# Optimization experiments

Measured on AMD Instinct MI355X. Metric: run time of the kernel, lower is better.

## Reference

```python
import jax, jax.numpy as jnp
import numpy as np
from functools import partial

# ---- constants from params ----
NODES = 64          # cfg_s[0]: nodes per graph
HEADS, BASES = 8, 4 # EGConv num_heads / num_bases (aggregators = ['symnorm'], A=1)
THRESH, LENS = 0.5, 0.5
ENC_THRESH, ENC_LENS = 0.5, 0.5
DECAY = 0.2
LSTM_ALPHA = 2.0

# ---- surrogate spike functions ----
@partial(jax.custom_vjp, nondiff_argnums=(1, 2))
def atan_spike(x, thresh, alpha):
    return (x > thresh).astype(x.dtype)

def _atan_fwd(x, thresh, alpha):
    return atan_spike(x, thresh, alpha), x

def _atan_bwd(thresh, alpha, x, g):
    grad = (alpha / 2.0) / (1.0 + (jnp.pi / 2.0 * alpha * (x - thresh)) ** 2)
    return (g * grad,)

atan_spike.defvjp(_atan_fwd, _atan_bwd)

@partial(jax.custom_vjp, nondiff_argnums=(1,))
def erf_spike(x, alpha):
    return (x > 0).astype(x.dtype)

def _erf_fwd(x, alpha):
    return erf_spike(x, alpha), x

def _erf_bwd(alpha, x, g):
    grad = alpha / (2.0 * jnp.sqrt(jnp.pi)) * jnp.exp(-(alpha * x / 2.0) ** 2)
    return (g * grad,)

erf_spike.defvjp(_erf_fwd, _erf_bwd)


def setup_inputs() -> dict:
    key = jax.random.key(0)
    N, Cin, T = 16384, 8, 32
    Cenc, Cgnn = 128, 128
    Fh = Cgnn // HEADS
    HID, FC1, NC = 512, 256, 4
    E = 262144
    ks = jax.random.split(key, 12)

    def w(k, shape, fan_in):
        return jax.random.normal(k, shape, jnp.float32) / np.float32(np.sqrt(fan_in))

    return {
        "x": jax.random.normal(ks[0], (N, Cin, T), jnp.float32),
        "edge_index": jax.random.randint(ks[1], (2, E), 0, N, dtype=jnp.int32),
        "enc_W": w(ks[2], (Cin, Cenc), Cin),
        "enc_b": jnp.zeros((Cenc,), jnp.float32),
        "bases_W": w(ks[3], (Cenc, BASES * Fh), Cenc),
        "bases_b": jnp.zeros((BASES * Fh,), jnp.float32),
        "comb_W": w(ks[4], (Cenc, HEADS * BASES), Cenc),
        "comb_b": jnp.zeros((HEADS * BASES,), jnp.float32),
        "conv_bias": jnp.zeros((Cgnn,), jnp.float32),
        "W_ih": w(ks[5], (NODES * Cgnn, 4 * HID), NODES * Cgnn),
        "W_hh": w(ks[6], (HID, 4 * HID), HID),
        "b_ih": jnp.zeros((4 * HID,), jnp.float32),
        "b_hh": jnp.zeros((4 * HID,), jnp.float32),
        "fc1_W": w(ks[7], (HID, FC1), HID),
        "fc1_b": jnp.zeros((FC1,), jnp.float32),
        "fc2_W": w(ks[8], (FC1, NC), FC1),
        "fc2_b": jnp.zeros((NC,), jnp.float32),
    }


def reference(x, edge_index, enc_W, enc_b, bases_W, bases_b, comb_W, comb_b,
              conv_bias, W_ih, W_hh, b_ih, b_hh, fc1_W, fc1_b, fc2_W, fc2_b):
    N, Cin, T = x.shape
    S = N // NODES
    Cgnn = conv_bias.shape[0]
    Fh = Cgnn // HEADS
    HID = W_hh.shape[0]
    FC1 = fc1_b.shape[0]
    NC = fc2_b.shape[0]

    # EGConv symnorm graph structure with self-loops (fixed across time)
    loop = jnp.arange(N, dtype=edge_index.dtype)
    s_all = jnp.concatenate([edge_index[0], loop])
    d_all = jnp.concatenate([edge_index[1], loop])
    deg = jax.ops.segment_sum(jnp.ones(s_all.shape[0], x.dtype), d_all, num_segments=N)
    dinv = jnp.where(deg > 0, jax.lax.rsqrt(jnp.maximum(deg, 1e-12)), 0.0)
    ew = dinv[s_all] * dinv[d_all]  # [E+N]

    xs = jnp.moveaxis(x, -1, 0)  # [T, N, Cin]

    def step(carry, xt):
        (enc_mem, enc_spike, c1_mem, c1_spike, lh, lc,
         h1_mem, h1_spike, h2_mem, h2_spike, h2_sum) = carry
        # encoding LIF
        enc_mem = enc_mem * DECAY * (1.0 - enc_spike) + xt @ enc_W + enc_b
        enc_spike = atan_spike(enc_mem, ENC_THRESH, ENC_LENS)
        # EGConv (symnorm aggregator, A=1)
        bases = enc_spike @ bases_W + bases_b                       # [N, B*Fh]
        agg = jax.ops.segment_sum(ew[:, None] * bases[s_all], d_all, num_segments=N)
        comb = (enc_spike @ comb_W + comb_b).reshape(N, HEADS, BASES)
        conv = jnp.einsum('nhb,nbf->nhf', comb, agg.reshape(N, BASES, Fh))
        conv = conv.reshape(S, NODES, Cgnn) + conv_bias
        # conv LIF
        c1_mem = c1_mem * DECAY * (1.0 - c1_spike) + conv
        c1_spike = atan_spike(c1_mem, THRESH, LENS)
        # spiking LSTM cell (erf surrogates on all gates)
        xl = c1_spike.reshape(S, NODES * Cgnn)
        gates = xl @ W_ih + b_ih + lh @ W_hh + b_hh
        i, f, g, o = jnp.split(gates, 4, axis=-1)
        i = erf_spike(i, LSTM_ALPHA)
        f = erf_spike(f, LSTM_ALPHA)
        g = erf_spike(g, LSTM_ALPHA)
        o = erf_spike(o, LSTM_ALPHA)
        lc = f * lc + i * g
        lh = lc * o
        # fc1 LIF
        h1_mem = h1_mem * DECAY * (1.0 - h1_spike) + lh @ fc1_W + fc1_b
        h1_spike = atan_spike(h1_mem, THRESH, LENS)
        # fc2 LIF
        h2_mem = h2_mem * DECAY * (1.0 - h2_spike) + h1_spike @ fc2_W + fc2_b
        h2_spike = atan_spike(h2_mem, THRESH, LENS)
        return (enc_mem, enc_spike, c1_mem, c1_spike, lh, lc,
                h1_mem, h1_spike, h2_mem, h2_spike, h2_sum + h2_spike), None

    Cenc = enc_b.shape[0]
    z = lambda shape: jnp.zeros(shape, x.dtype)
    carry0 = (z((N, Cenc)), z((N, Cenc)), z((S, NODES, Cgnn)), z((S, NODES, Cgnn)),
              z((S, HID)), z((S, HID)), z((S, FC1)), z((S, FC1)),
              z((S, NC)), z((S, NC)), z((S, NC)))
    carry, _ = jax.lax.scan(step, carry0, xs)
    h2_sum = carry[-1]
    return h2_sum / jnp.asarray(T, x.dtype)
```

## Files before the change

### kernel.cpp

```cpp
#include <hip/hip_runtime.h>

#define NN      16384
#define TSTEPS  32
#define SG      256
#define NE      262144
#define NPANEL  24
#define GSTRIDE 524288u

#define OFF_ENC_MEM   0u
#define OFF_ENC_SPK   2097152u
#define OFF_C1_MEM    4194304u
#define OFF_C1_SPK    6291456u
#define OFF_LH        8388608u
#define OFF_LC        8519680u
#define OFF_H1_MEM    8650752u
#define OFF_H1_SPK    8716288u
#define OFF_H2_MEM    8781824u
#define OFF_H2_SPK    8782848u
#define OFF_H2_SUM    8783872u
#define ZERO_FLOATS   8784896u
#define OFF_BASES     8784896u
#define OFF_COMB      9833472u
#define OFF_GATES     10357760u
#define OFF_PART      10882048u
#define OFF_DINV      23464960u
#define OFF_COLW      23481344u
#define FLOAT_END     23743488u
#define IOFF_DEG      0
#define IOFF_FILL     16384
#define IOFF_ROWPTR   32768
#define IOFF_EID      49153
#define IOFF_COL      311297
#define INT_COUNT     573441

__global__ void k_deg(const int* __restrict__ ei, int* __restrict__ deg) {
  int e = blockIdx.x * 256 + threadIdx.x;
  if (e < NE) atomicAdd(&deg[ei[NE + e]], 1);
}

__global__ void k_dinv(const int* __restrict__ deg, float* __restrict__ dinv) {
  int n = blockIdx.x * 256 + threadIdx.x;
  if (n < NN) dinv[n] = __fdiv_rn(1.0f, __fsqrt_rn((float)(deg[n] + 1)));
}

__global__ void k_scan(const int* __restrict__ deg, int* __restrict__ rowp) {
  __shared__ int sdata[1024];
  int tid = threadIdx.x;
  int base = tid * 16;
  int loc[16];
  int sum = 0;
  #pragma unroll
  for (int i = 0; i < 16; ++i) { loc[i] = sum; sum += deg[base + i]; }
  sdata[tid] = sum;
  __syncthreads();
  for (int off = 1; off < 1024; off <<= 1) {
    int v = 0;
    if (tid >= off) v = sdata[tid - off];
    __syncthreads();
    sdata[tid] += v;
    __syncthreads();
  }
  int excl = (tid == 0) ? 0 : sdata[tid - 1];
  #pragma unroll
  for (int i = 0; i < 16; ++i) rowp[base + i] = excl + loc[i];
  if (tid == 1023) rowp[NN] = sdata[1023];
}

__global__ void k_scatter(const int* __restrict__ ei, const int* __restrict__ rowp,
                          int* __restrict__ fill, int* __restrict__ eid) {
  int e = blockIdx.x * 256 + threadIdx.x;
  if (e >= NE) return;
  int d = ei[NE + e];
  int pos = rowp[d] + atomicAdd(&fill[d], 1);
  eid[pos] = e;
}

__global__ void k_sortadj(const int* __restrict__ rowp, int* __restrict__ eid,
                          const int* __restrict__ ei, const float* __restrict__ dinv,
                          int* __restrict__ col, float* __restrict__ colw) {
  int d = blockIdx.x * 256 + threadIdx.x;
  if (d >= NN) return;
  int r0 = rowp[d], r1 = rowp[d + 1];
  for (int i = r0 + 1; i < r1; ++i) {
    int key = eid[i];
    int j = i - 1;
    while (j >= r0 && eid[j] > key) { eid[j + 1] = eid[j]; --j; }
    eid[j + 1] = key;
  }
  for (int i = r0; i < r1; ++i) {
    int s = ei[eid[i]];
    col[i] = s;
    colw[i] = dinv[s];
  }
}

__global__ __launch_bounds__(256) void k_enc(
    const float* __restrict__ x, const float* __restrict__ encW, const float* __restrict__ encB,
    float* __restrict__ enc_mem, float* __restrict__ enc_spk, int t) {
  __shared__ float xs[2][8];
  int tid = threadIdx.x;
  int nb = blockIdx.x * 2;
  if (tid < 16)
    xs[tid >> 3][tid & 7] = x[(size_t)(nb + (tid >> 3)) * 256 + (size_t)(tid & 7) * 32 + t];
  __syncthreads();
  int nl = tid >> 7, j = tid & 127;
  int idx = (nb + nl) * 128 + j;
  float dot = 0.f;
  #pragma unroll
  for (int c = 0; c < 8; ++c) dot = __fmaf_rn(xs[nl][c], encW[c * 128 + j], dot);
  float m = enc_mem[idx], s = enc_spk[idx];
  float nm = __fadd_rn(__fadd_rn(__fmul_rn(__fmul_rn(m, 0.2f), __fsub_rn(1.f, s)), dot), encB[j]);
  enc_mem[idx] = nm;
  enc_spk[idx] = nm > 0.5f ? 1.f : 0.f;
}

__global__ __launch_bounds__(256) void k_bases_comb(
    const float* __restrict__ enc_spk,
    const float* __restrict__ basesW, const float* __restrict__ basesB,
    const float* __restrict__ combW, const float* __restrict__ combB,
    float* __restrict__ bases, float* __restrict__ comb) {
  __shared__ float sp[64 * 129];
  __shared__ float ob[64 * 65];
  __shared__ float oc[64 * 33];
  const int tid = threadIdx.x;
  const int nb = blockIdx.x * 64;
  #pragma unroll 4
  for (int k = 0; k < 32; ++k) {
    int idx = k * 256 + tid;
    int n = idx >> 7, j = idx & 127;
    sp[n * 129 + j] = enc_spk[(size_t)nb * 128 + idx];
  }
  __syncthreads();
  const int lane = tid & 63;
  const int w = tid >> 6;
  const float* spn = sp + lane * 129;
  if (w < 2) {
    const int ch0 = w * 32;
    const float* Wp = basesW + ch0;
    float acc[32];
    #pragma unroll
    for (int c = 0; c < 32; ++c) acc[c] = 0.f;
    for (int j = 0; j < 128; ++j) {
      const float s = spn[j];
      const float* wr = Wp + j * 64;
      #pragma unroll
      for (int c = 0; c < 32; ++c) acc[c] = __fmaf_rn(s, wr[c], acc[c]);
    }
    #pragma unroll
    for (int c = 0; c < 32; ++c) ob[lane * 65 + ch0 + c] = acc[c];
  } else {
    const int ch0 = (w - 2) * 16;
    const float* Wp = combW + ch0;
    float acc[16];
    #pragma unroll
    for (int c = 0; c < 16; ++c) acc[c] = 0.f;
    for (int j = 0; j < 128; ++j) {
      const float s = spn[j];
      const float* wr = Wp + j * 32;
      #pragma unroll
      for (int c = 0; c < 16; ++c) acc[c] = __fmaf_rn(s, wr[c], acc[c]);
    }
    #pragma unroll
    for (int c = 0; c < 16; ++c) oc[lane * 33 + ch0 + c] = acc[c];
  }
  __syncthreads();
  #pragma unroll
  for (int r = 0; r < 16; ++r) {
    int idx = r * 256 + tid;
    int n = idx >> 6, ch = idx & 63;
    bases[(size_t)(nb + n) * 64 + ch] = __fadd_rn(ob[n * 65 + ch], basesB[ch]);
  }
  #pragma unroll
  for (int r = 0; r < 8; ++r) {
    int idx = r * 256 + tid;
    int n = idx >> 5, ch = idx & 31;
    comb[(size_t)(nb + n) * 32 + ch] = __fadd_rn(oc[n * 33 + ch], combB[ch]);
  }
}

__global__ __launch_bounds__(256) void k_aggconv(
    const float* __restrict__ bases, const float* __restrict__ comb,
    const float* __restrict__ dinv, const int* __restrict__ rowp,
    const int* __restrict__ col, const float* __restrict__ colw,
    const float* __restrict__ convB,
    float* __restrict__ c1_mem, float* __restrict__ c1_spk) {
  __shared__ float aggl[4][64];
  __shared__ float combl[4][32];
  int w = threadIdx.x >> 6;
  int m = threadIdx.x & 63;
  int d = blockIdx.x * 4 + w;
  float dd = dinv[d];
  int r0 = rowp[d], r1 = rowp[d + 1];
  float acc = 0.f;
  for (int r = r0; r < r1; ++r) {
    int s = col[r];
    float ew  = __fmul_rn(colw[r], dd);
    float upd = __fmul_rn(ew, bases[(size_t)s * 64 + m]);
    acc = __fadd_rn(acc, upd);
  }
  {
    float ew  = __fmul_rn(dd, dd);
    float upd = __fmul_rn(ew, bases[(size_t)d * 64 + m]);
    acc = __fadd_rn(acc, upd);
  }
  aggl[w][m] = acc;
  if (m < 32) combl[w][m] = comb[(size_t)d * 32 + m];
  __syncthreads();
  #pragma unroll
  for (int half = 0; half < 2; ++half) {
    int j = m + half * 64;
    int h = j >> 4, f = j & 15;
    float cv = 0.f;
    #pragma unroll
    for (int b = 0; b < 4; ++b)
      cv = __fadd_rn(cv, __fmul_rn(combl[w][h * 4 + b], aggl[w][b * 16 + f]));
    cv = __fadd_rn(cv, convB[j]);
    int idx = d * 128 + j;
    float cm = c1_mem[idx], cs = c1_spk[idx];
    float nm = __fadd_rn(__fmul_rn(__fmul_rn(cm, 0.2f), __fsub_rn(1.f, cs)), cv);
    c1_mem[idx] = nm;
    c1_spk[idx] = nm > 0.5f ? 1.f : 0.f;
  }
}

__global__ __launch_bounds__(256) void k_gpanel(
    const float* __restrict__ xl, const float* __restrict__ lh,
    const float* __restrict__ Wih, const float* __restrict__ Whh,
    float* __restrict__ part) {
  __shared__ __align__(16) float Ast[16][132];
  __shared__ __align__(16) float Bs[16][132];
  const int tid = threadIdx.x;
  const int tx = tid & 15, ty = tid >> 4;
  const int n0 = blockIdx.x * 128;
  const int m0 = blockIdx.y * 128;
  const int z  = blockIdx.z;

  const float* Asrc; const float* Bsrc; int lda, k0, klen;
  if (z < 22) { Asrc = xl; Bsrc = Wih; lda = 8192; k0 = z * 384; klen = (z == 21) ? 128 : 384; }
  else        { Asrc = lh; Bsrc = Whh; lda = 512;  k0 = (z == 22) ? 0 : 384; klen = (z == 22) ? 384 : 128; }

  float acc[8][8];
  #pragma unroll
  for (int i = 0; i < 8; ++i)
    #pragma unroll
    for (int j = 0; j < 8; ++j) acc[i][j] = 0.f;

  const int arow = tid >> 1;
  const int acol = (tid & 1) * 8;
  const int brow = tid >> 5;
  const int bcol = (tid & 31) * 4;

  const int nkt = klen >> 4;
  for (int kt = 0; kt < nkt; ++kt) {
    const int kb = k0 + (kt << 4);
    __syncthreads();
    {
      const float* src = Asrc + (size_t)(m0 + arow) * lda + kb + acol;
      const float4 v0 = ((const float4*)src)[0];
      const float4 v1 = ((const float4*)src)[1];
      Ast[acol + 0][arow] = v0.x; Ast[acol + 1][arow] = v0.y;
      Ast[acol + 2][arow] = v0.z; Ast[acol + 3][arow] = v0.w;
      Ast[acol + 4][arow] = v1.x; Ast[acol + 5][arow] = v1.y;
      Ast[acol + 6][arow] = v1.z; Ast[acol + 7][arow] = v1.w;
    }
    {
      *(float4*)&Bs[brow][bcol] =
          *(const float4*)(Bsrc + (size_t)(kb + brow) * 2048 + n0 + bcol);
      *(float4*)&Bs[brow + 8][bcol] =
          *(const float4*)(Bsrc + (size_t)(kb + brow + 8) * 2048 + n0 + bcol);
    }
    __syncthreads();
    #pragma unroll
    for (int kk = 0; kk < 16; ++kk) {
      const float4 a0 = *(const float4*)&Ast[kk][ty * 4];
      const float4 a1 = *(const float4*)&Ast[kk][64 + ty * 4];
      const float4 b0 = *(const float4*)&Bs[kk][tx * 4];
      const float4 b1 = *(const float4*)&Bs[kk][64 + tx * 4];
      const float av[8] = {a0.x, a0.y, a0.z, a0.w, a1.x, a1.y, a1.z, a1.w};
      const float bv[8] = {b0.x, b0.y, b0.z, b0.w, b1.x, b1.y, b1.z, b1.w};
      #pragma unroll
      for (int i = 0; i < 8; ++i)
        #pragma unroll
        for (int j = 0; j < 8; ++j)
          acc[i][j] = __fmaf_rn(av[i], bv[j], acc[i][j]);
    }
  }
  float* dstz = part + (size_t)z * GSTRIDE + (size_t)m0 * 2048 + n0;
  #pragma unroll
  for (int i = 0; i < 8; ++i) {
    const int mr = ((i >> 2) << 6) + ty * 4 + (i & 3);
    float* row = dstz + (size_t)mr * 2048;
    *(float4*)(row + tx * 4)      = make_float4(acc[i][0], acc[i][1], acc[i][2], acc[i][3]);
    *(float4*)(row + 64 + tx * 4) = make_float4(acc[i][4], acc[i][5], acc[i][6], acc[i][7]);
  }
}

__global__ __launch_bounds__(256) void k_combine(
    const float* __restrict__ part, const float* __restrict__ bih,
    const float* __restrict__ bhh, float* __restrict__ gates) {
  const int idx = blockIdx.x * 256 + threadIdx.x;
  const float* p = part + idx;
  float tih = p[0];
  #pragma unroll
  for (int zz = 1; zz < 22; ++zz) tih = __fadd_rn(tih, p[(size_t)zz * GSTRIDE]);
  const float thh = __fadd_rn(p[22u * GSTRIDE], p[23u * GSTRIDE]);
  const int u = idx & 2047;
  gates[idx] = __fadd_rn(__fadd_rn(__fadd_rn(tih, bih[u]), thh), bhh[u]);
}

__global__ __launch_bounds__(256) void k_cell(
    const float* __restrict__ gates,
    float* __restrict__ lc, float* __restrict__ lh,
    const float* __restrict__ fc1W, const float* __restrict__ fc1b,
    const float* __restrict__ fc2W, const float* __restrict__ fc2b,
    float* __restrict__ h1_mem, float* __restrict__ h1_spk,
    float* __restrict__ h2_mem, float* __restrict__ h2_spk, float* __restrict__ h2_sum) {
  __shared__ float lhl[512];
  __shared__ float sp1l[256];
  const int s = blockIdx.x;
  const int p = threadIdx.x;
  #pragma unroll
  for (int half = 0; half < 2; ++half) {
    const int h = p + half * 256;
    const float giv = gates[(size_t)s * 2048 + h];
    const float gfv = gates[(size_t)s * 2048 + 512 + h];
    const float ggv = gates[(size_t)s * 2048 + 1024 + h];
    const float gov = gates[(size_t)s * 2048 + 1536 + h];
    const float iv = giv > 0.f ? 1.f : 0.f;
    const float fv = gfv > 0.f ? 1.f : 0.f;
    const float gv = ggv > 0.f ? 1.f : 0.f;
    const float ov = gov > 0.f ? 1.f : 0.f;
    const int li = s * 512 + h;
    const float lcv = __fadd_rn(__fmul_rn(fv, lc[li]), __fmul_rn(iv, gv));
    lc[li] = lcv;
    const float lhv = __fmul_rn(lcv, ov);
    lh[li] = lhv;
    lhl[h] = lhv;
  }
  __syncthreads();
  float a0 = 0.f, a1 = 0.f;
  #pragma unroll 8
  for (int q = 0; q < 384; ++q) a0 = __fmaf_rn(lhl[q], fc1W[q * 256 + p], a0);
  #pragma unroll 8
  for (int q = 384; q < 512; ++q) a1 = __fmaf_rn(lhl[q], fc1W[q * 256 + p], a1);
  const float dot1 = __fadd_rn(a0, a1);
  const int i1 = s * 256 + p;
  const float m1 = h1_mem[i1], s1o = h1_spk[i1];
  const float nm1 = __fadd_rn(__fadd_rn(__fmul_rn(__fmul_rn(m1, 0.2f), __fsub_rn(1.f, s1o)), dot1), fc1b[p]);
  h1_mem[i1] = nm1;
  const float sp1 = nm1 > 0.5f ? 1.f : 0.f;
  h1_spk[i1] = sp1;
  sp1l[p] = sp1;
  __syncthreads();
  if (p < 4) {
    float acc = 0.f;
    for (int q = 0; q < 256; ++q) acc = __fmaf_rn(sp1l[q], fc2W[q * 4 + p], acc);
    const int i2 = s * 4 + p;
    const float m2 = h2_mem[i2], s2o = h2_spk[i2];
    const float nm2 = __fadd_rn(__fadd_rn(__fmul_rn(__fmul_rn(m2, 0.2f), __fsub_rn(1.f, s2o)), acc), fc2b[p]);
    h2_mem[i2] = nm2;
    const float sp2 = nm2 > 0.5f ? 1.f : 0.f;
    h2_spk[i2] = sp2;
    h2_sum[i2] = __fadd_rn(h2_sum[i2], sp2);
  }
}

__global__ void k_out(const float* __restrict__ h2_sum, float* __restrict__ out) {
  int i = blockIdx.x * 256 + threadIdx.x;
  if (i < SG * 4) out[i] = __fmul_rn(h2_sum[i], 0.03125f);
}

extern "C" void kernel_launch(void* const* d_in, const int* in_sizes, int n_in,
                              void* d_out, int out_size, void* d_ws, size_t ws_size,
                              hipStream_t stream) {
  const float* x      = (const float*)d_in[0];
  const int*   ei     = (const int*)  d_in[1];
  const float* encW   = (const float*)d_in[2];
  const float* encB   = (const float*)d_in[3];
  const float* basesW = (const float*)d_in[4];
  const float* basesB = (const float*)d_in[5];
  const float* combW  = (const float*)d_in[6];
  const float* combB  = (const float*)d_in[7];
  const float* convB  = (const float*)d_in[8];
  const float* Wih    = (const float*)d_in[9];
  const float* Whh    = (const float*)d_in[10];
  const float* bih    = (const float*)d_in[11];
  const float* bhh    = (const float*)d_in[12];
  const float* fc1W   = (const float*)d_in[13];
  const float* fc1b   = (const float*)d_in[14];
  const float* fc2W   = (const float*)d_in[15];
  const float* fc2b   = (const float*)d_in[16];

  float* ws = (float*)d_ws;
  float* enc_mem = ws + OFF_ENC_MEM;
  float* enc_spk = ws + OFF_ENC_SPK;
  float* c1_mem  = ws + OFF_C1_MEM;
  float* c1_spk  = ws + OFF_C1_SPK;
  float* lhp     = ws + OFF_LH;
  float* lcp     = ws + OFF_LC;
  float* h1_mem  = ws + OFF_H1_MEM;
  float* h1_spk  = ws + OFF_H1_SPK;
  float* h2_mem  = ws + OFF_H2_MEM;
  float* h2_spk  = ws + OFF_H2_SPK;
  float* h2_sum  = ws + OFF_H2_SUM;
  float* bases   = ws + OFF_BASES;
  float* comb    = ws + OFF_COMB;
  float* gates   = ws + OFF_GATES;
  float* partp   = ws + OFF_PART;
  float* dinv    = ws + OFF_DINV;
  float* colw    = ws + OFF_COLW;
  int* ibase = (int*)((char*)d_ws + (size_t)FLOAT_END * 4);
  int* deg  = ibase + IOFF_DEG;
  int* fill = ibase + IOFF_FILL;
  int* rowp = ibase + IOFF_ROWPTR;
  int* eid  = ibase + IOFF_EID;
  int* col  = ibase + IOFF_COL;

  hipMemsetAsync(ws, 0, (size_t)ZERO_FLOATS * 4, stream);
  hipMemsetAsync(ibase, 0, 32768 * 4, stream);

  k_deg    <<<NE / 256, 256, 0, stream>>>(ei, deg);
  k_dinv   <<<NN / 256, 256, 0, stream>>>(deg, dinv);
  k_scan   <<<1, 1024, 0, stream>>>(deg, rowp);
  k_scatter<<<NE / 256, 256, 0, stream>>>(ei, rowp, fill, eid);
  k_sortadj<<<NN / 256, 256, 0, stream>>>(rowp, eid, ei, dinv, col, colw);

  for (int t = 0; t < TSTEPS; ++t) {
    k_enc       <<<NN / 2, 256, 0, stream>>>(x, encW, encB, enc_mem, enc_spk, t);
    k_bases_comb<<<NN / 64, 256, 0, stream>>>(enc_spk, basesW, basesB, combW, combB, bases, comb);
    k_aggconv   <<<NN / 4, 256, 0, stream>>>(bases, comb, dinv, rowp, col, colw, convB, c1_mem, c1_spk);
    k_gpanel    <<<dim3(16, 2, NPANEL), 256, 0, stream>>>(c1_spk, lhp, Wih, Whh, partp);
    k_combine   <<<2048, 256, 0, stream>>>(partp, bih, bhh, gates);
    k_cell      <<<SG, 256, 0, stream>>>(gates, lcp, lhp, fc1W, fc1b, fc2W, fc2b,
                                         h1_mem, h1_spk, h2_mem, h2_spk, h2_sum);
  }
  k_out<<<4, 256, 0, stream>>>(h2_sum, (float*)d_out);
}
```

Measured before the change: 7.066 ms.

## Shrink gate GEMM tile width and fuse split-K reduction into LSTM cell kernel

```diff
diff --git a/kernel.cpp b/kernel.cpp
--- a/kernel.cpp
+++ b/kernel.cpp
@@ -223,15 +223,15 @@
   }
 }
 
-__global__ __launch_bounds__(256) void k_gpanel(
+__global__ __launch_bounds__(256, 4) void k_gpanel(
     const float* __restrict__ xl, const float* __restrict__ lh,
     const float* __restrict__ Wih, const float* __restrict__ Whh,
     float* __restrict__ part) {
   __shared__ __align__(16) float Ast[16][132];
-  __shared__ __align__(16) float Bs[16][132];
+  __shared__ __align__(16) float Bs[16][68];
   const int tid = threadIdx.x;
   const int tx = tid & 15, ty = tid >> 4;
-  const int n0 = blockIdx.x * 128;
+  const int n0 = blockIdx.x * 64;
   const int m0 = blockIdx.y * 128;
   const int z  = blockIdx.z;
 
@@ -239,16 +239,16 @@
   if (z < 22) { Asrc = xl; Bsrc = Wih; lda = 8192; k0 = z * 384; klen = (z == 21) ? 128 : 384; }
   else        { Asrc = lh; Bsrc = Whh; lda = 512;  k0 = (z == 22) ? 0 : 384; klen = (z == 22) ? 384 : 128; }
 
-  float acc[8][8];
+  float acc[8][4];
   #pragma unroll
   for (int i = 0; i < 8; ++i)
     #pragma unroll
-    for (int j = 0; j < 8; ++j) acc[i][j] = 0.f;
+    for (int j = 0; j < 4; ++j) acc[i][j] = 0.f;
 
   const int arow = tid >> 1;
   const int acol = (tid & 1) * 8;
-  const int brow = tid >> 5;
-  const int bcol = (tid & 31) * 4;
+  const int brow = tid >> 4;
+  const int bcol = (tid & 15) * 4;
 
   const int nkt = klen >> 4;
   for (int kt = 0; kt < nkt; ++kt) {
@@ -266,8 +266,6 @@
     {
       *(float4*)&Bs[brow][bcol] =
           *(const float4*)(Bsrc + (size_t)(kb + brow) * 2048 + n0 + bcol);
-      *(float4*)&Bs[brow + 8][bcol] =
-          *(const float4*)(Bsrc + (size_t)(kb + brow + 8) * 2048 + n0 + bcol);
     }
     __syncthreads();
     #pragma unroll
@@ -275,13 +273,12 @@
       const float4 a0 = *(const float4*)&Ast[kk][ty * 4];
       const float4 a1 = *(const float4*)&Ast[kk][64 + ty * 4];
       const float4 b0 = *(const float4*)&Bs[kk][tx * 4];
-      const float4 b1 = *(const float4*)&Bs[kk][64 + tx * 4];
       const float av[8] = {a0.x, a0.y, a0.z, a0.w, a1.x, a1.y, a1.z, a1.w};
-      const float bv[8] = {b0.x, b0.y, b0.z, b0.w, b1.x, b1.y, b1.z, b1.w};
+      const float bv[4] = {b0.x, b0.y, b0.z, b0.w};
       #pragma unroll
       for (int i = 0; i < 8; ++i)
         #pragma unroll
-        for (int j = 0; j < 8; ++j)
+        for (int j = 0; j < 4; ++j)
           acc[i][j] = __fmaf_rn(av[i], bv[j], acc[i][j]);
     }
   }
@@ -289,27 +286,13 @@
   #pragma unroll
   for (int i = 0; i < 8; ++i) {
     const int mr = ((i >> 2) << 6) + ty * 4 + (i & 3);
-    float* row = dstz + (size_t)mr * 2048;
-    *(float4*)(row + tx * 4)      = make_float4(acc[i][0], acc[i][1], acc[i][2], acc[i][3]);
-    *(float4*)(row + 64 + tx * 4) = make_float4(acc[i][4], acc[i][5], acc[i][6], acc[i][7]);
-  }
-}
-
-__global__ __launch_bounds__(256) void k_combine(
-    const float* __restrict__ part, const float* __restrict__ bih,
-    const float* __restrict__ bhh, float* __restrict__ gates) {
-  const int idx = blockIdx.x * 256 + threadIdx.x;
-  const float* p = part + idx;
-  float tih = p[0];
-  #pragma unroll
-  for (int zz = 1; zz < 22; ++zz) tih = __fadd_rn(tih, p[(size_t)zz * GSTRIDE]);
-  const float thh = __fadd_rn(p[22u * GSTRIDE], p[23u * GSTRIDE]);
-  const int u = idx & 2047;
-  gates[idx] = __fadd_rn(__fadd_rn(__fadd_rn(tih, bih[u]), thh), bhh[u]);
+    *(float4*)(dstz + (size_t)mr * 2048 + tx * 4) =
+        make_float4(acc[i][0], acc[i][1], acc[i][2], acc[i][3]);
+  }
 }
 
 __global__ __launch_bounds__(256) void k_cell(
-    const float* __restrict__ gates,
+    const float* __restrict__ part, const float* __restrict__ bih, const float* __restrict__ bhh,
     float* __restrict__ lc, float* __restrict__ lh,
     const float* __restrict__ fc1W, const float* __restrict__ fc1b,
     const float* __restrict__ fc2W, const float* __restrict__ fc2b,
@@ -322,16 +305,23 @@
   #pragma unroll
   for (int half = 0; half < 2; ++half) {
     const int h = p + half * 256;
-    const float giv = gates[(size_t)s * 2048 + h];
-    const float gfv = gates[(size_t)s * 2048 + 512 + h];
-    const float ggv = gates[(size_t)s * 2048 + 1024 + h];
-    const float gov = gates[(size_t)s * 2048 + 1536 + h];
-    const float iv = giv > 0.f ? 1.f : 0.f;
-    const float fv = gfv > 0.f ? 1.f : 0.f;
-    const float gv = ggv > 0.f ? 1.f : 0.f;
-    const float ov = gov > 0.f ? 1.f : 0.f;
+    float gv[4];
+    #pragma unroll
+    for (int g = 0; g < 4; ++g) {
+      const int u = g * 512 + h;
+      const float* pp = part + (size_t)s * 2048 + u;
+      float tih = pp[0];
+      #pragma unroll
+      for (int zz = 1; zz < 22; ++zz) tih = __fadd_rn(tih, pp[(size_t)zz * GSTRIDE]);
+      const float thh = __fadd_rn(pp[22u * GSTRIDE], pp[23u * GSTRIDE]);
+      gv[g] = __fadd_rn(__fadd_rn(__fadd_rn(tih, bih[u]), thh), bhh[u]);
+    }
+    const float iv = gv[0] > 0.f ? 1.f : 0.f;
+    const float fv = gv[1] > 0.f ? 1.f : 0.f;
+    const float ggv = gv[2] > 0.f ? 1.f : 0.f;
+    const float ov = gv[3] > 0.f ? 1.f : 0.f;
     const int li = s * 512 + h;
-    const float lcv = __fadd_rn(__fmul_rn(fv, lc[li]), __fmul_rn(iv, gv));
+    const float lcv = __fadd_rn(__fmul_rn(fv, lc[li]), __fmul_rn(iv, ggv));
     lc[li] = lcv;
     const float lhv = __fmul_rn(lcv, ov);
     lh[li] = lhv;
@@ -405,7 +395,6 @@
   float* h2_sum  = ws + OFF_H2_SUM;
   float* bases   = ws + OFF_BASES;
   float* comb    = ws + OFF_COMB;
-  float* gates   = ws + OFF_GATES;
   float* partp   = ws + OFF_PART;
   float* dinv    = ws + OFF_DINV;
   float* colw    = ws + OFF_COLW;
@@ -429,9 +418,8 @@
     k_enc       <<<NN / 2, 256, 0, stream>>>(x, encW, encB, enc_mem, enc_spk, t);
     k_bases_comb<<<NN / 64, 256, 0, stream>>>(enc_spk, basesW, basesB, combW, combB, bases, comb);
     k_aggconv   <<<NN / 4, 256, 0, stream>>>(bases, comb, dinv, rowp, col, colw, convB, c1_mem, c1_spk);
-    k_gpanel    <<<dim3(16, 2, NPANEL), 256, 0, stream>>>(c1_spk, lhp, Wih, Whh, partp);
-    k_combine   <<<2048, 256, 0, stream>>>(partp, bih, bhh, gates);
-    k_cell      <<<SG, 256, 0, stream>>>(gates, lcp, lhp, fc1W, fc1b, fc2W, fc2b,
+    k_gpanel    <<<dim3(32, 2, NPANEL), 256, 0, stream>>>(c1_spk, lhp, Wih, Whh, partp);
+    k_cell      <<<SG, 256, 0, stream>>>(partp, bih, bhh, lcp, lhp, fc1W, fc1b, fc2W, fc2b,
                                          h1_mem, h1_spk, h2_mem, h2_spk, h2_sum);
   }
   k_out<<<4, 256, 0, stream>>>(h2_sum, (float*)d_out);
```

Result: slower. 7.225 ms (+2.3%).

## Fuse encoder LIF into bases/comb kernel and shrink GEMM per-thread tile

Applied to the files above, without the earlier changes.

```diff
diff --git a/kernel.cpp b/kernel.cpp
--- a/kernel.cpp
+++ b/kernel.cpp
@@ -94,41 +94,39 @@
   }
 }
 
-__global__ __launch_bounds__(256) void k_enc(
+__global__ __launch_bounds__(256) void k_bases_comb(
     const float* __restrict__ x, const float* __restrict__ encW, const float* __restrict__ encB,
-    float* __restrict__ enc_mem, float* __restrict__ enc_spk, int t) {
-  __shared__ float xs[2][8];
-  int tid = threadIdx.x;
-  int nb = blockIdx.x * 2;
-  if (tid < 16)
-    xs[tid >> 3][tid & 7] = x[(size_t)(nb + (tid >> 3)) * 256 + (size_t)(tid & 7) * 32 + t];
-  __syncthreads();
-  int nl = tid >> 7, j = tid & 127;
-  int idx = (nb + nl) * 128 + j;
-  float dot = 0.f;
-  #pragma unroll
-  for (int c = 0; c < 8; ++c) dot = __fmaf_rn(xs[nl][c], encW[c * 128 + j], dot);
-  float m = enc_mem[idx], s = enc_spk[idx];
-  float nm = __fadd_rn(__fadd_rn(__fmul_rn(__fmul_rn(m, 0.2f), __fsub_rn(1.f, s)), dot), encB[j]);
-  enc_mem[idx] = nm;
-  enc_spk[idx] = nm > 0.5f ? 1.f : 0.f;
-}
-
-__global__ __launch_bounds__(256) void k_bases_comb(
-    const float* __restrict__ enc_spk,
+    float* __restrict__ enc_mem, float* __restrict__ enc_spk,
     const float* __restrict__ basesW, const float* __restrict__ basesB,
     const float* __restrict__ combW, const float* __restrict__ combB,
-    float* __restrict__ bases, float* __restrict__ comb) {
+    float* __restrict__ bases, float* __restrict__ comb, int t) {
+  __shared__ float xs[64][8];
   __shared__ float sp[64 * 129];
   __shared__ float ob[64 * 65];
   __shared__ float oc[64 * 33];
   const int tid = threadIdx.x;
   const int nb = blockIdx.x * 64;
+  #pragma unroll
+  for (int k = 0; k < 2; ++k) {
+    int idx = k * 256 + tid;
+    int n = idx >> 3, c = idx & 7;
+    xs[n][c] = x[(size_t)(nb + n) * 256 + (size_t)c * 32 + t];
+  }
+  __syncthreads();
   #pragma unroll 4
   for (int k = 0; k < 32; ++k) {
     int idx = k * 256 + tid;
     int n = idx >> 7, j = idx & 127;
-    sp[n * 129 + j] = enc_spk[(size_t)nb * 128 + idx];
+    int gidx = nb * 128 + idx;
+    float dot = 0.f;
+    #pragma unroll
+    for (int c = 0; c < 8; ++c) dot = __fmaf_rn(xs[n][c], encW[c * 128 + j], dot);
+    float m = enc_mem[gidx], s = enc_spk[gidx];
+    float nm = __fadd_rn(__fadd_rn(__fmul_rn(__fmul_rn(m, 0.2f), __fsub_rn(1.f, s)), dot), encB[j]);
+    enc_mem[gidx] = nm;
+    float spk = nm > 0.5f ? 1.f : 0.f;
+    enc_spk[gidx] = spk;
+    sp[n * 129 + j] = spk;
   }
   __syncthreads();
   const int lane = tid & 63;
@@ -223,14 +221,15 @@
   }
 }
 
-__global__ __launch_bounds__(256) void k_gpanel(
+__global__ __launch_bounds__(512) void k_gpanel(
     const float* __restrict__ xl, const float* __restrict__ lh,
     const float* __restrict__ Wih, const float* __restrict__ Whh,
     float* __restrict__ part) {
   __shared__ __align__(16) float Ast[16][132];
   __shared__ __align__(16) float Bs[16][132];
   const int tid = threadIdx.x;
-  const int tx = tid & 15, ty = tid >> 4;
+  const int tx = tid & 31;
+  const int ty = tid >> 5;
   const int n0 = blockIdx.x * 128;
   const int m0 = blockIdx.y * 128;
   const int z  = blockIdx.z;
@@ -239,14 +238,14 @@
   if (z < 22) { Asrc = xl; Bsrc = Wih; lda = 8192; k0 = z * 384; klen = (z == 21) ? 128 : 384; }
   else        { Asrc = lh; Bsrc = Whh; lda = 512;  k0 = (z == 22) ? 0 : 384; klen = (z == 22) ? 384 : 128; }
 
-  float acc[8][8];
+  float acc[8][4];
   #pragma unroll
   for (int i = 0; i < 8; ++i)
     #pragma unroll
-    for (int j = 0; j < 8; ++j) acc[i][j] = 0.f;
-
-  const int arow = tid >> 1;
-  const int acol = (tid & 1) * 8;
+    for (int j = 0; j < 4; ++j) acc[i][j] = 0.f;
+
+  const int arow = tid >> 2;
+  const int acol = (tid & 3) * 4;
   const int brow = tid >> 5;
   const int bcol = (tid & 31) * 4;
 
@@ -255,43 +254,35 @@
     const int kb = k0 + (kt << 4);
     __syncthreads();
     {
-      const float* src = Asrc + (size_t)(m0 + arow) * lda + kb + acol;
-      const float4 v0 = ((const float4*)src)[0];
-      const float4 v1 = ((const float4*)src)[1];
-      Ast[acol + 0][arow] = v0.x; Ast[acol + 1][arow] = v0.y;
-      Ast[acol + 2][arow] = v0.z; Ast[acol + 3][arow] = v0.w;
-      Ast[acol + 4][arow] = v1.x; Ast[acol + 5][arow] = v1.y;
-      Ast[acol + 6][arow] = v1.z; Ast[acol + 7][arow] = v1.w;
+      const float4 va = *(const float4*)(Asrc + (size_t)(m0 + arow) * lda + kb + acol);
+      Ast[acol + 0][arow] = va.x; Ast[acol + 1][arow] = va.y;
+      Ast[acol + 2][arow] = va.z; Ast[acol + 3][arow] = va.w;
     }
     {
       *(float4*)&Bs[brow][bcol] =
           *(const float4*)(Bsrc + (size_t)(kb + brow) * 2048 + n0 + bcol);
-      *(float4*)&Bs[brow + 8][bcol] =
-          *(const float4*)(Bsrc + (size_t)(kb + brow + 8) * 2048 + n0 + bcol);
     }
     __syncthreads();
     #pragma unroll
     for (int kk = 0; kk < 16; ++kk) {
-      const float4 a0 = *(const float4*)&Ast[kk][ty * 4];
-      const float4 a1 = *(const float4*)&Ast[kk][64 + ty * 4];
+      const float4 a0 = *(const float4*)&Ast[kk][ty * 8];
+      const float4 a1 = *(const float4*)&Ast[kk][ty * 8 + 4];
       const float4 b0 = *(const float4*)&Bs[kk][tx * 4];
-      const float4 b1 = *(const float4*)&Bs[kk][64 + tx * 4];
       const float av[8] = {a0.x, a0.y, a0.z, a0.w, a1.x, a1.y, a1.z, a1.w};
-      const float bv[8] = {b0.x, b0.y, b0.z, b0.w, b1.x, b1.y, b1.z, b1.w};
+      const float bv[4] = {b0.x, b0.y, b0.z, b0.w};
       #pragma unroll
       for (int i = 0; i < 8; ++i)
         #pragma unroll
-        for (int j = 0; j < 8; ++j)
+        for (int j = 0; j < 4; ++j)
           acc[i][j] = __fmaf_rn(av[i], bv[j], acc[i][j]);
     }
   }
   float* dstz = part + (size_t)z * GSTRIDE + (size_t)m0 * 2048 + n0;
   #pragma unroll
   for (int i = 0; i < 8; ++i) {
-    const int mr = ((i >> 2) << 6) + ty * 4 + (i & 3);
-    float* row = dstz + (size_t)mr * 2048;
-    *(float4*)(row + tx * 4)      = make_float4(acc[i][0], acc[i][1], acc[i][2], acc[i][3]);
-    *(float4*)(row + 64 + tx * 4) = make_float4(acc[i][4], acc[i][5], acc[i][6], acc[i][7]);
+    const int mr = ty * 8 + i;
+    *(float4*)(dstz + (size_t)mr * 2048 + tx * 4) =
+        make_float4(acc[i][0], acc[i][1], acc[i][2], acc[i][3]);
   }
 }
 
@@ -426,10 +417,10 @@
   k_sortadj<<<NN / 256, 256, 0, stream>>>(rowp, eid, ei, dinv, col, colw);
 
   for (int t = 0; t < TSTEPS; ++t) {
-    k_enc       <<<NN / 2, 256, 0, stream>>>(x, encW, encB, enc_mem, enc_spk, t);
-    k_bases_comb<<<NN / 64, 256, 0, stream>>>(enc_spk, basesW, basesB, combW, combB, bases, comb);
+    k_bases_comb<<<NN / 64, 256, 0, stream>>>(x, encW, encB, enc_mem, enc_spk,
+                                              basesW, basesB, combW, combB, bases, comb, t);
     k_aggconv   <<<NN / 4, 256, 0, stream>>>(bases, comb, dinv, rowp, col, colw, convB, c1_mem, c1_spk);
-    k_gpanel    <<<dim3(16, 2, NPANEL), 256, 0, stream>>>(c1_spk, lhp, Wih, Whh, partp);
+    k_gpanel    <<<dim3(16, 2, NPANEL), 512, 0, stream>>>(c1_spk, lhp, Wih, Whh, partp);
     k_combine   <<<2048, 256, 0, stream>>>(partp, bih, bhh, gates);
     k_cell      <<<SG, 256, 0, stream>>>(gates, lcp, lhp, fc1W, fc1b, fc2W, fc2b,
                                          h1_mem, h1_spk, h2_mem, h2_spk, h2_sum);
```

Result: no change. 6.936 ms (-1.8%).
